# Kernel optimization log

Measured on AMD Instinct MI355X. Metric: run time of the kernel, lower is better.

The kernel has to match this reference:

```python
import jax, jax.numpy as jnp
import numpy as np

N_NODES = 50000
N_EDGES = 400000
NODE_DIM = 128
EDGE_DIM = 64
HIDDEN = 128  # must equal NODE_DIM (index_add into zeros_like(node_feat))
EPS = 1e-8


def _param(key, shape):
    fan_in = shape[0]
    return (jax.random.normal(key, shape, jnp.float32) / np.sqrt(fan_in)).astype(jnp.float32)


def setup_inputs() -> dict:
    key = jax.random.key(0)
    ks = jax.random.split(key, 20)
    inp = {
        'node_feat': jax.random.normal(ks[0], (N_NODES, NODE_DIM), jnp.float32),
        'edge_attr': jax.random.normal(ks[1], (N_EDGES, EDGE_DIM), jnp.float32),
        'coords': 5.0 * jax.random.normal(ks[2], (N_NODES, 3), jnp.float32),
        'edge_index': jax.random.randint(ks[3], (2, N_EDGES), 0, N_NODES, dtype=jnp.int32),
        # edge_mlp: Linear(2*node+edge -> hidden), SiLU, Linear(hidden -> hidden), SiLU
        'We1': _param(ks[4], (2 * NODE_DIM + EDGE_DIM, HIDDEN)),
        'be1': jnp.zeros((HIDDEN,), jnp.float32),
        'We2': _param(ks[5], (HIDDEN, HIDDEN)),
        'be2': jnp.zeros((HIDDEN,), jnp.float32),
        # node_mlp: Linear(node+hidden -> hidden), SiLU, Linear(hidden -> node)
        'Wn1': _param(ks[6], (NODE_DIM + HIDDEN, HIDDEN)),
        'bn1': jnp.zeros((HIDDEN,), jnp.float32),
        'Wn2': _param(ks[7], (HIDDEN, NODE_DIM)),
        'bn2': jnp.zeros((NODE_DIM,), jnp.float32),
        # coord_mlp: Linear(hidden -> hidden//2), SiLU, Linear(hidden//2 -> 1)
        'Wc1': _param(ks[8], (HIDDEN, HIDDEN // 2)),
        'bc1': jnp.zeros((HIDDEN // 2,), jnp.float32),
        'Wc2': _param(ks[9], (HIDDEN // 2, 1)),
        'bc2': jnp.zeros((1,), jnp.float32),
    }
    return inp


def reference(node_feat, edge_attr, coords, edge_index,
              We1, be1, We2, be2,
              Wn1, bn1, Wn2, bn2,
              Wc1, bc1, Wc2, bc2):
    src, dst = edge_index[0], edge_index[1]
    n_nodes = node_feat.shape[0]

    # gather -> edge MLP
    edge_feat = jnp.concatenate([node_feat[src], node_feat[dst], edge_attr], axis=-1)  # [E, 2*ND+ED]
    edge_message = jax.nn.silu(jax.nn.silu(edge_feat @ We1 + be1) @ We2 + be2)         # [E, H]

    # scatter-add messages to destination nodes
    aggr = jax.ops.segment_sum(edge_message, dst, num_segments=n_nodes)                # [N, H]

    # node update (residual)
    node_in = jnp.concatenate([node_feat, aggr], axis=-1)
    node_update = jax.nn.silu(node_in @ Wn1 + bn1) @ Wn2 + bn2
    updated_nodes = node_feat + node_update

    # equivariant coordinate update
    coord_w = jax.nn.silu(edge_message @ Wc1 + bc1) @ Wc2 + bc2                        # [E, 1]
    coord_diff = coords[src] - coords[dst]                                             # [E, 3]
    coord_diff = coord_diff / (jnp.linalg.norm(coord_diff, axis=-1, keepdims=True) + EPS)
    coord_update = jax.ops.segment_sum(coord_w * coord_diff, dst, num_segments=n_nodes)
    updated_coords = coords + coord_update

    return (updated_nodes, updated_coords)
```

## Files before the change

### kernel.cpp

```cpp
#include <hip/hip_runtime.h>
#include <hip/hip_bf16.h>
#include <math.h>
#include <stdint.h>

#define NN 50000
#define NE 400000

typedef __attribute__((ext_vector_type(8))) short short8;
typedef __attribute__((ext_vector_type(4))) float f32x4;

#define OFF_W1S  0
#define OFF_W1D  16384
#define OFF_W1E  32768
#define OFF_WE2T 40960
#define OFF_WN1T 57344
#define OFF_WN2T 90112
#define OFF_WC1T 106496
#define W_TOTAL  114688

__device__ __forceinline__ float silu_f(float x) {
    return x * (1.0f / (1.0f + __expf(-x)));
}
__device__ __forceinline__ short f2bf(float f) {
    __hip_bfloat16 b = __float2bfloat16(f);
    return *reinterpret_cast<short*>(&b);
}
__device__ __forceinline__ float bf2f(short s) {
    uint32_t u = ((uint32_t)(uint16_t)s) << 16;
    float f; __builtin_memcpy(&f, &u, 4); return f;
}
__device__ __forceinline__ short8 cvt8(float4 a, float4 b) {
    short8 r;
    r[0] = f2bf(a.x); r[1] = f2bf(a.y); r[2] = f2bf(a.z); r[3] = f2bf(a.w);
    r[4] = f2bf(b.x); r[5] = f2bf(b.y); r[6] = f2bf(b.z); r[7] = f2bf(b.w);
    return r;
}

__device__ __forceinline__ void gload16(const short* g, short* l) {
    __builtin_amdgcn_global_load_lds(
        (const __attribute__((address_space(1))) void*)g,
        (__attribute__((address_space(3))) void*)l, 16, 0, 0);
}

__global__ void zero_kernel(float4* __restrict__ p, int n4) {
    int i = blockIdx.x * blockDim.x + threadIdx.x;
    int st = gridDim.x * blockDim.x;
    for (; i < n4; i += st) p[i] = make_float4(0.f, 0.f, 0.f, 0.f);
}

__global__ __launch_bounds__(256) void prep_kernel(
    const float* __restrict__ We1, const float* __restrict__ We2,
    const float* __restrict__ Wn1, const float* __restrict__ Wn2,
    const float* __restrict__ Wc1, short* __restrict__ wb)
{
    const int i = blockIdx.x * 256 + threadIdx.x;
    if (i >= W_TOTAL) return;
    float v; int rel, n, k;
    if (i < OFF_W1D)       { rel = i;            n = rel >> 7; k = rel & 127; v = We1[k * 128 + n]; }
    else if (i < OFF_W1E)  { rel = i - OFF_W1D;  n = rel >> 7; k = rel & 127; v = We1[(k + 128) * 128 + n]; }
    else if (i < OFF_WE2T) { rel = i - OFF_W1E;  n = rel >> 6; k = rel & 63;  v = We1[(k + 256) * 128 + n]; }
    else if (i < OFF_WN1T) { rel = i - OFF_WE2T; n = rel >> 7; k = rel & 127; v = We2[k * 128 + n]; }
    else if (i < OFF_WN2T) { rel = i - OFF_WN1T; n = rel >> 8; k = rel & 255; v = Wn1[k * 128 + n]; }
    else if (i < OFF_WC1T) { rel = i - OFF_WN2T; n = rel >> 7; k = rel & 127; v = Wn2[k * 128 + n]; }
    else                   { rel = i - OFF_WC1T; n = rel >> 7; k = rel & 127; v = Wc1[k * 64 + n]; }
    wb[i] = f2bf(v);
}

__global__ __launch_bounds__(256, 4) void ynode_kernel(
    const float* __restrict__ nf, const short* __restrict__ wb,
    short* __restrict__ ysb, short* __restrict__ ydb)
{
    const int tid = threadIdx.x;
    const int wv = tid >> 6, lane = tid & 63, le = lane & 15, grp = lane >> 4;
    const int nb = blockIdx.x * 128, wbase = wv * 32;
    const int row0 = min(nb + wbase + le, NN - 1);
    const int row1 = min(nb + wbase + 16 + le, NN - 1);

    #pragma unroll 1
    for (int pass = 0; pass < 2; ++pass) {
        const short* wt = wb + (pass ? OFF_W1D : OFF_W1S);
        short* op = pass ? ydb : ysb;

        f32x4 acc[2][8];
        #pragma unroll
        for (int m = 0; m < 2; ++m)
            #pragma unroll
            for (int t = 0; t < 8; ++t) acc[m][t] = (f32x4){0.f, 0.f, 0.f, 0.f};

        #pragma unroll
        for (int kc = 0; kc < 4; ++kc) {
            const int gk = kc * 32 + grp * 8;
            const float* p0 = nf + (size_t)row0 * 128 + gk;
            const float* p1 = nf + (size_t)row1 * 128 + gk;
            const short8 a0 = cvt8(*(const float4*)p0, *(const float4*)(p0 + 4));
            const short8 a1 = cvt8(*(const float4*)p1, *(const float4*)(p1 + 4));
            short8 bfv[8];
            #pragma unroll
            for (int t = 0; t < 8; ++t)
                bfv[t] = *(const short8*)(wt + (size_t)(t * 16 + le) * 128 + gk);
            #pragma unroll
            for (int t = 0; t < 8; ++t) {
                acc[0][t] = __builtin_amdgcn_mfma_f32_16x16x32_bf16(a0, bfv[t], acc[0][t], 0, 0, 0);
                acc[1][t] = __builtin_amdgcn_mfma_f32_16x16x32_bf16(a1, bfv[t], acc[1][t], 0, 0, 0);
            }
        }
        #pragma unroll
        for (int t = 0; t < 8; ++t)
            #pragma unroll
            for (int m = 0; m < 2; ++m)
                #pragma unroll
                for (int r = 0; r < 4; ++r) {
                    const int row = nb + wbase + m * 16 + grp * 4 + r;
                    if (row < NN)
                        op[(size_t)row * 128 + t * 16 + le] = f2bf(acc[m][t][r]);
                }
    }
}

__global__ __launch_bounds__(256, 2) void edge_kernel(
    const short* __restrict__ ysb, const short* __restrict__ ydb,
    const float* __restrict__ ea, const float* __restrict__ coords,
    const int* __restrict__ ei, const short* __restrict__ wb,
    const float* __restrict__ be1, const float* __restrict__ be2,
    const float* __restrict__ bc1, const float* __restrict__ bc2,
    const float* __restrict__ Wc2f,
    float* __restrict__ aggr, float* __restrict__ coord_acc)
{
    __shared__ short smem[4][8192];

    const int tid = threadIdx.x;
    const int wv = tid >> 6, lane = tid & 63, le = lane & 15, g = lane >> 4;
    const int base = (blockIdx.x * 4 + wv) * 32;
    short* stage = smem[wv];

    const int s0 = ei[base + le],      s1 = ei[base + 16 + le];
    const int d0 = ei[NE + base + le], d1 = ei[NE + base + 16 + le];

    #pragma unroll
    for (int q = 0; q < 4; ++q) {
        gload16(ysb + (size_t)s0 * 128 + q * 32 + g * 8, stage + q * 512);
        gload16(ysb + (size_t)s1 * 128 + q * 32 + g * 8, stage + 2048 + q * 512);
        gload16(ydb + (size_t)d0 * 128 + q * 32 + g * 8, stage + 4096 + q * 512);
        gload16(ydb + (size_t)d1 * 128 + q * 32 + g * 8, stage + 6144 + q * 512);
    }

    f32x4 acc[2][8];
    #pragma unroll
    for (int m = 0; m < 2; ++m)
        #pragma unroll
        for (int t = 0; t < 8; ++t) acc[m][t] = (f32x4){0.f, 0.f, 0.f, 0.f};

    const short* w1e = wb + OFF_W1E;
    #pragma unroll
    for (int kc = 0; kc < 2; ++kc) {
        const int gk = kc * 32 + g * 8;
        const float* p0 = ea + (size_t)(base + le) * 64 + gk;
        const float* p1 = ea + (size_t)(base + 16 + le) * 64 + gk;
        const short8 a0 = cvt8(*(const float4*)p0, *(const float4*)(p0 + 4));
        const short8 a1 = cvt8(*(const float4*)p1, *(const float4*)(p1 + 4));
        short8 bfv[8];
        #pragma unroll
        for (int t = 0; t < 8; ++t)
            bfv[t] = *(const short8*)(w1e + (size_t)(t * 16 + le) * 64 + gk);
        #pragma unroll
        for (int t = 0; t < 8; ++t) {
            acc[0][t] = __builtin_amdgcn_mfma_f32_16x16x32_bf16(a0, bfv[t], acc[0][t], 0, 0, 0);
            acc[1][t] = __builtin_amdgcn_mfma_f32_16x16x32_bf16(a1, bfv[t], acc[1][t], 0, 0, 0);
        }
    }

    asm volatile("s_waitcnt vmcnt(0)" ::: "memory");
    __builtin_amdgcn_sched_barrier(0);

    #pragma unroll
    for (int t = 0; t < 8; ++t) {
        const int col = t * 16 + le;
        const float b1 = be1[col];
        const int c8 = col >> 3, q = c8 >> 2, cc = c8 & 3, el = col & 7;
        #pragma unroll
        for (int m = 0; m < 2; ++m)
            #pragma unroll
            for (int r = 0; r < 4; ++r) {
                const int ad = m * 2048 + q * 512 + cc * 128 + (g * 4 + r) * 8 + el;
                const float v = silu_f(acc[m][t][r] + bf2f(stage[ad]) + bf2f(stage[4096 + ad]) + b1);
                stage[ad] = f2bf(v);
            }
    }

    f32x4 acc2[2][8];
    #pragma unroll
    for (int m = 0; m < 2; ++m)
        #pragma unroll
        for (int t = 0; t < 8; ++t) acc2[m][t] = (f32x4){0.f, 0.f, 0.f, 0.f};

    const short* w2 = wb + OFF_WE2T;
    #pragma unroll
    for (int kc = 0; kc < 4; ++kc) {
        const int gk = kc * 32 + g * 8;
        const short8 a0 = *(const short8*)&stage[kc * 512 + g * 128 + le * 8];
        const short8 a1 = *(const short8*)&stage[2048 + kc * 512 + g * 128 + le * 8];
        short8 bfv[8];
        #pragma unroll
        for (int t = 0; t < 8; ++t)
            bfv[t] = *(const short8*)(w2 + (size_t)(t * 16 + le) * 128 + gk);
        #pragma unroll
        for (int t = 0; t < 8; ++t) {
            acc2[0][t] = __builtin_amdgcn_mfma_f32_16x16x32_bf16(a0, bfv[t], acc2[0][t], 0, 0, 0);
            acc2[1][t] = __builtin_amdgcn_mfma_f32_16x16x32_bf16(a1, bfv[t], acc2[1][t], 0, 0, 0);
        }
    }

    int dstv[2][4];
    #pragma unroll
    for (int r = 0; r < 4; ++r) {
        dstv[0][r] = __shfl(d0, g * 4 + r);
        dstv[1][r] = __shfl(d1, g * 4 + r);
    }
    #pragma unroll
    for (int t = 0; t < 8; ++t) {
        const int col = t * 16 + le;
        const float b2 = be2[col];
        const int c8 = col >> 3, q = c8 >> 2, cc = c8 & 3, el = col & 7;
        #pragma unroll
        for (int m = 0; m < 2; ++m)
            #pragma unroll
            for (int r = 0; r < 4; ++r) {
                const float v = silu_f(acc2[m][t][r] + b2);
                atomicAdd(&aggr[(size_t)dstv[m][r] * 128 + col], v);
                stage[4096 + m * 2048 + q * 512 + cc * 128 + (g * 4 + r) * 8 + el] = f2bf(v);
            }
    }

    f32x4 acc3[2][4];
    #pragma unroll
    for (int m = 0; m < 2; ++m)
        #pragma unroll
        for (int t = 0; t < 4; ++t) acc3[m][t] = (f32x4){0.f, 0.f, 0.f, 0.f};

    const short* wc = wb + OFF_WC1T;
    #pragma unroll
    for (int kc = 0; kc < 4; ++kc) {
        const int gk = kc * 32 + g * 8;
        const short8 a0 = *(const short8*)&stage[4096 + kc * 512 + g * 128 + le * 8];
        const short8 a1 = *(const short8*)&stage[6144 + kc * 512 + g * 128 + le * 8];
        short8 bfv[4];
        #pragma unroll
        for (int t = 0; t < 4; ++t)
            bfv[t] = *(const short8*)(wc + (size_t)(t * 16 + le) * 128 + gk);
        #pragma unroll
        for (int t = 0; t < 4; ++t) {
            acc3[0][t] = __builtin_amdgcn_mfma_f32_16x16x32_bf16(a0, bfv[t], acc3[0][t], 0, 0, 0);
            acc3[1][t] = __builtin_amdgcn_mfma_f32_16x16x32_bf16(a1, bfv[t], acc3[1][t], 0, 0, 0);
        }
    }

    float part[2][4];
    #pragma unroll
    for (int m = 0; m < 2; ++m)
        #pragma unroll
        for (int r = 0; r < 4; ++r) part[m][r] = 0.f;
    #pragma unroll
    for (int t = 0; t < 4; ++t) {
        const float bc = bc1[t * 16 + le];
        const float w2c = Wc2f[t * 16 + le];
        #pragma unroll
        for (int m = 0; m < 2; ++m)
            #pragma unroll
            for (int r = 0; r < 4; ++r)
                part[m][r] += silu_f(acc3[m][t][r] + bc) * w2c;
    }
    #pragma unroll
    for (int mask = 1; mask <= 8; mask <<= 1)
        #pragma unroll
        for (int m = 0; m < 2; ++m)
            #pragma unroll
            for (int r = 0; r < 4; ++r)
                part[m][r] += __shfl_xor(part[m][r], mask);

    const int rr = le & 3;
    const int sA = __shfl(s0, g * 4 + rr), sB = __shfl(s1, g * 4 + rr);
    const int dA = __shfl(d0, g * 4 + rr), dB = __shfl(d1, g * 4 + rr);

    if (le < 8) {
        const int m = le >> 2, r = le & 3;
        float v;
        if (m == 0) v = (r == 0) ? part[0][0] : (r == 1) ? part[0][1] : (r == 2) ? part[0][2] : part[0][3];
        else        v = (r == 0) ? part[1][0] : (r == 1) ? part[1][1] : (r == 2) ? part[1][2] : part[1][3];
        const int s = m ? sB : sA, d = m ? dB : dA;
        const float dx = coords[3 * s + 0] - coords[3 * d + 0];
        const float dy = coords[3 * s + 1] - coords[3 * d + 1];
        const float dz = coords[3 * s + 2] - coords[3 * d + 2];
        const float wq = v + bc2[0];
        const float inv = wq / (sqrtf(dx * dx + dy * dy + dz * dz) + 1e-8f);
        atomicAdd(&coord_acc[3 * d + 0], dx * inv);
        atomicAdd(&coord_acc[3 * d + 1], dy * inv);
        atomicAdd(&coord_acc[3 * d + 2], dz * inv);
    }
}

__global__ __launch_bounds__(256, 2) void node_kernel(
    const float* __restrict__ nf, const float* __restrict__ coords,
    const short* __restrict__ wb,
    const float* __restrict__ bn1, const float* __restrict__ bn2,
    const float* __restrict__ aggr, const float* __restrict__ coord_acc,
    float* __restrict__ out)
{
    __shared__ short Hs[128][136];

    const int tid = threadIdx.x;
    const int wv = tid >> 6, lane = tid & 63, le = lane & 15, grp = lane >> 4;
    const int nb = blockIdx.x * 128, wbase = wv * 32;
    const int row0 = min(nb + wbase + le, NN - 1);
    const int row1 = min(nb + wbase + 16 + le, NN - 1);

    f32x4 acc[2][8];
    #pragma unroll
    for (int m = 0; m < 2; ++m)
        #pragma unroll
        for (int t = 0; t < 8; ++t) acc[m][t] = (f32x4){0.f, 0.f, 0.f, 0.f};

    const short* w1 = wb + OFF_WN1T;
    #pragma unroll
    for (int kc = 0; kc < 8; ++kc) {
        const int gk = kc * 32 + grp * 8;
        const float* p0 = (kc < 4) ? nf + (size_t)row0 * 128 + gk : aggr + (size_t)row0 * 128 + gk - 128;
        const float* p1 = (kc < 4) ? nf + (size_t)row1 * 128 + gk : aggr + (size_t)row1 * 128 + gk - 128;
        const short8 a0 = cvt8(*(const float4*)p0, *(const float4*)(p0 + 4));
        const short8 a1 = cvt8(*(const float4*)p1, *(const float4*)(p1 + 4));
        short8 bfv[8];
        #pragma unroll
        for (int t = 0; t < 8; ++t)
            bfv[t] = *(const short8*)(w1 + (size_t)(t * 16 + le) * 256 + gk);
        #pragma unroll
        for (int t = 0; t < 8; ++t) {
            acc[0][t] = __builtin_amdgcn_mfma_f32_16x16x32_bf16(a0, bfv[t], acc[0][t], 0, 0, 0);
            acc[1][t] = __builtin_amdgcn_mfma_f32_16x16x32_bf16(a1, bfv[t], acc[1][t], 0, 0, 0);
        }
    }
    #pragma unroll
    for (int t = 0; t < 8; ++t) {
        const float b1 = bn1[t * 16 + le];
        #pragma unroll
        for (int m = 0; m < 2; ++m)
            #pragma unroll
            for (int r = 0; r < 4; ++r)
                Hs[wbase + m * 16 + grp * 4 + r][t * 16 + le] = f2bf(silu_f(acc[m][t][r] + b1));
    }

    f32x4 acc2[2][8];
    #pragma unroll
    for (int m = 0; m < 2; ++m)
        #pragma unroll
        for (int t = 0; t < 8; ++t) acc2[m][t] = (f32x4){0.f, 0.f, 0.f, 0.f};

    const short* w2 = wb + OFF_WN2T;
    #pragma unroll
    for (int kc = 0; kc < 4; ++kc) {
        const int gk = kc * 32 + grp * 8;
        const short8 a0 = *(const short8*)&Hs[wbase + le][gk];
        const short8 a1 = *(const short8*)&Hs[wbase + 16 + le][gk];
        short8 bfv[8];
        #pragma unroll
        for (int t = 0; t < 8; ++t)
            bfv[t] = *(const short8*)(w2 + (size_t)(t * 16 + le) * 128 + gk);
        #pragma unroll
        for (int t = 0; t < 8; ++t) {
            acc2[0][t] = __builtin_amdgcn_mfma_f32_16x16x32_bf16(a0, bfv[t], acc2[0][t], 0, 0, 0);
            acc2[1][t] = __builtin_amdgcn_mfma_f32_16x16x32_bf16(a1, bfv[t], acc2[1][t], 0, 0, 0);
        }
    }
    #pragma unroll
    for (int t = 0; t < 8; ++t) {
        const float b2 = bn2[t * 16 + le];
        #pragma unroll
        for (int m = 0; m < 2; ++m)
            #pragma unroll
            for (int r = 0; r < 4; ++r) {
                const int row = nb + wbase + m * 16 + grp * 4 + r;
                if (row < NN) {
                    const int c = t * 16 + le;
                    out[(size_t)row * 128 + c] = acc2[m][t][r] + b2 + nf[(size_t)row * 128 + c];
                }
            }
    }

    for (int i = tid; i < 384; i += 256) {
        const int n = nb + i / 3, j = i % 3;
        if (n < NN)
            out[(size_t)NN * 128 + 3 * n + j] = coords[3 * n + j] + coord_acc[3 * n + j];
    }
}

extern "C" void kernel_launch(void* const* d_in, const int* in_sizes, int n_in,
                              void* d_out, int out_size, void* d_ws, size_t ws_size,
                              hipStream_t stream)
{
    const float* node_feat  = (const float*)d_in[0];
    const float* edge_attr  = (const float*)d_in[1];
    const float* coords     = (const float*)d_in[2];
    const int*   edge_index = (const int*)d_in[3];
    const float* We1 = (const float*)d_in[4];
    const float* be1 = (const float*)d_in[5];
    const float* We2 = (const float*)d_in[6];
    const float* be2 = (const float*)d_in[7];
    const float* Wn1 = (const float*)d_in[8];
    const float* bn1 = (const float*)d_in[9];
    const float* Wn2 = (const float*)d_in[10];
    const float* bn2 = (const float*)d_in[11];
    const float* Wc1 = (const float*)d_in[12];
    const float* bc1 = (const float*)d_in[13];
    const float* Wc2 = (const float*)d_in[14];
    const float* bc2 = (const float*)d_in[15];
    float* out = (float*)d_out;

    const size_t sz_wb  = (size_t)W_TOTAL * 2;
    const size_t sz_agg = (size_t)NN * 128 * 4;
    const size_t sz_cac = (size_t)NN * 3 * 4;
    const size_t sz_y   = (size_t)NN * 128 * 2;

    char* p = (char*)d_ws;
    short* wbf       = (short*)p;  p += sz_wb;
    float* aggr      = (float*)p;  p += sz_agg;
    float* coord_acc = (float*)p;  p += sz_cac;
    short* ysb       = (short*)p;  p += sz_y;
    short* ydb       = (short*)p;
    (void)ws_size;

    const int n4 = (NN * 128 + NN * 3) / 4;
    const int eg = NE / 128;
    const int ng = (NN + 127) / 128;

    prep_kernel<<<(W_TOTAL + 255) / 256, 256, 0, stream>>>(We1, We2, Wn1, Wn2, Wc1, wbf);
    zero_kernel<<<2048, 256, 0, stream>>>((float4*)aggr, n4);
    ynode_kernel<<<ng, 256, 0, stream>>>(node_feat, wbf, ysb, ydb);

    edge_kernel<<<eg, 256, 0, stream>>>(
        ysb, ydb, edge_attr, coords, edge_index, wbf,
        be1, be2, bc1, bc2, Wc2, aggr, coord_acc);

    node_kernel<<<ng, 256, 0, stream>>>(
        node_feat, coords, wbf, bn1, bn2, aggr, coord_acc, out);
}
```

Baseline: 390.0 us.

## Rewrite edge kernel as register-only transposed MFMA with shuffle exchange, no LDS

The edge kernel now computes the transposed product (weights as the A operand, edge features as B), so each lane owns the columns of one edge. Intermediate activations are passed between the chained matmuls through cross-lane shuffles instead of a shared-memory staging buffer. Each wave now handles 16 edges instead of 32, the grid doubles, and launch bounds allow 4 blocks per SM, removing the LDS round-trips and raising occupancy. The costs are more shuffle instructions, half the reuse of each weight fragment per wave, and aggr atomics that now land on a single destination row per lane with a changed column pattern.

```diff
diff --git a/kernel.cpp b/kernel.cpp
--- a/kernel.cpp
+++ b/kernel.cpp
@@ -29,6 +29,9 @@
     uint32_t u = ((uint32_t)(uint16_t)s) << 16;
     float f; __builtin_memcpy(&f, &u, 4); return f;
 }
+__device__ __forceinline__ uint32_t pk2(float lo, float hi) {
+    return (uint32_t)(uint16_t)f2bf(lo) | ((uint32_t)(uint16_t)f2bf(hi) << 16);
+}
 __device__ __forceinline__ short8 cvt8(float4 a, float4 b) {
     short8 r;
     r[0] = f2bf(a.x); r[1] = f2bf(a.y); r[2] = f2bf(a.z); r[3] = f2bf(a.w);
@@ -36,10 +39,20 @@
     return r;
 }
 
-__device__ __forceinline__ void gload16(const short* g, short* l) {
-    __builtin_amdgcn_global_load_lds(
-        (const __attribute__((address_space(1))) void*)g,
-        (__attribute__((address_space(3))) void*)l, 16, 0, 0);
+__device__ __forceinline__ short8 exch8(uint32_t e0, uint32_t e1,
+                                        uint32_t o0, uint32_t o1,
+                                        int g, int le) {
+    const int srcA = le + 16 * ((g & 1) * 2);
+    const int srcB = srcA + 16;
+    const uint32_t a0e = __shfl((int)e0, srcA), a0o = __shfl((int)o0, srcA);
+    const uint32_t a1e = __shfl((int)e1, srcA), a1o = __shfl((int)o1, srcA);
+    const uint32_t b0e = __shfl((int)e0, srcB), b0o = __shfl((int)o0, srcB);
+    const uint32_t b1e = __shfl((int)e1, srcB), b1o = __shfl((int)o1, srcB);
+    const bool hi = (g & 2) != 0;
+    uint32_t v[4];
+    v[0] = hi ? a0o : a0e;  v[1] = hi ? a1o : a1e;
+    v[2] = hi ? b0o : b0e;  v[3] = hi ? b1o : b1e;
+    short8 r; __builtin_memcpy(&r, v, 16); return r;
 }
 
 __global__ void zero_kernel(float4* __restrict__ p, int n4) {
@@ -117,7 +130,7 @@
     }
 }
 
-__global__ __launch_bounds__(256, 2) void edge_kernel(
+__global__ __launch_bounds__(256, 4) void edge_kernel(
     const short* __restrict__ ysb, const short* __restrict__ ydb,
     const float* __restrict__ ea, const float* __restrict__ coords,
     const int* __restrict__ ei, const short* __restrict__ wb,
@@ -126,175 +139,134 @@
     const float* __restrict__ Wc2f,
     float* __restrict__ aggr, float* __restrict__ coord_acc)
 {
-    __shared__ short smem[4][8192];
-
     const int tid = threadIdx.x;
     const int wv = tid >> 6, lane = tid & 63, le = lane & 15, g = lane >> 4;
-    const int base = (blockIdx.x * 4 + wv) * 32;
-    short* stage = smem[wv];
-
-    const int s0 = ei[base + le],      s1 = ei[base + 16 + le];
-    const int d0 = ei[NE + base + le], d1 = ei[NE + base + 16 + le];
-
-    #pragma unroll
-    for (int q = 0; q < 4; ++q) {
-        gload16(ysb + (size_t)s0 * 128 + q * 32 + g * 8, stage + q * 512);
-        gload16(ysb + (size_t)s1 * 128 + q * 32 + g * 8, stage + 2048 + q * 512);
-        gload16(ydb + (size_t)d0 * 128 + q * 32 + g * 8, stage + 4096 + q * 512);
-        gload16(ydb + (size_t)d1 * 128 + q * 32 + g * 8, stage + 6144 + q * 512);
-    }
-
-    f32x4 acc[2][8];
-    #pragma unroll
-    for (int m = 0; m < 2; ++m)
-        #pragma unroll
-        for (int t = 0; t < 8; ++t) acc[m][t] = (f32x4){0.f, 0.f, 0.f, 0.f};
+    const int e = (blockIdx.x * 4 + wv) * 16 + le;
+
+    const int s0 = ei[e], d0 = ei[NE + e];
+
+    short8 ys8[4], yd8[4];
+    #pragma unroll
+    for (int cc = 0; cc < 4; ++cc) {
+        ys8[cc] = *(const short8*)(ysb + (size_t)s0 * 128 + cc * 32 + g * 8);
+        yd8[cc] = *(const short8*)(ydb + (size_t)d0 * 128 + cc * 32 + g * 8);
+    }
+
+    short8 eaB[2];
+    #pragma unroll
+    for (int kc = 0; kc < 2; ++kc) {
+        const float* pe = ea + (size_t)e * 64 + kc * 32 + g * 8;
+        eaB[kc] = cvt8(*(const float4*)pe, *(const float4*)(pe + 4));
+    }
+
+    f32x4 acc[8];
+    #pragma unroll
+    for (int t = 0; t < 8; ++t) acc[t] = (f32x4){0.f, 0.f, 0.f, 0.f};
 
     const short* w1e = wb + OFF_W1E;
     #pragma unroll
     for (int kc = 0; kc < 2; ++kc) {
         const int gk = kc * 32 + g * 8;
-        const float* p0 = ea + (size_t)(base + le) * 64 + gk;
-        const float* p1 = ea + (size_t)(base + 16 + le) * 64 + gk;
-        const short8 a0 = cvt8(*(const float4*)p0, *(const float4*)(p0 + 4));
-        const short8 a1 = cvt8(*(const float4*)p1, *(const float4*)(p1 + 4));
-        short8 bfv[8];
-        #pragma unroll
-        for (int t = 0; t < 8; ++t)
-            bfv[t] = *(const short8*)(w1e + (size_t)(t * 16 + le) * 64 + gk);
-        #pragma unroll
-        for (int t = 0; t < 8; ++t) {
-            acc[0][t] = __builtin_amdgcn_mfma_f32_16x16x32_bf16(a0, bfv[t], acc[0][t], 0, 0, 0);
-            acc[1][t] = __builtin_amdgcn_mfma_f32_16x16x32_bf16(a1, bfv[t], acc[1][t], 0, 0, 0);
+        short8 wfv[8];
+        #pragma unroll
+        for (int t = 0; t < 8; ++t)
+            wfv[t] = *(const short8*)(w1e + (size_t)(t * 16 + le) * 64 + gk);
+        #pragma unroll
+        for (int t = 0; t < 8; ++t)
+            acc[t] = __builtin_amdgcn_mfma_f32_16x16x32_bf16(wfv[t], eaB[kc], acc[t], 0, 0, 0);
+    }
+
+    uint32_t hp[8][2];
+    #pragma unroll
+    for (int t = 0; t < 8; ++t) {
+        hp[t][0] = pk2(acc[t][0], acc[t][1]);
+        hp[t][1] = pk2(acc[t][2], acc[t][3]);
+    }
+
+    short8 h1f[4];
+    #pragma unroll
+    for (int cc = 0; cc < 4; ++cc) {
+        const short8 ex = exch8(hp[cc*2][0], hp[cc*2][1], hp[cc*2+1][0], hp[cc*2+1][1], g, le);
+        const float* bp = be1 + cc * 32 + g * 8;
+        #pragma unroll
+        for (int j = 0; j < 8; ++j)
+            h1f[cc][j] = f2bf(silu_f(bf2f(ex[j]) + bf2f(ys8[cc][j]) + bf2f(yd8[cc][j]) + bp[j]));
+    }
+
+    f32x4 acc2[8];
+    #pragma unroll
+    for (int t = 0; t < 8; ++t) acc2[t] = (f32x4){0.f, 0.f, 0.f, 0.f};
+
+    const short* w2 = wb + OFF_WE2T;
+    #pragma unroll
+    for (int cc = 0; cc < 4; ++cc) {
+        const int gk = cc * 32 + g * 8;
+        short8 wfv[8];
+        #pragma unroll
+        for (int t = 0; t < 8; ++t)
+            wfv[t] = *(const short8*)(w2 + (size_t)(t * 16 + le) * 128 + gk);
+        #pragma unroll
+        for (int t = 0; t < 8; ++t)
+            acc2[t] = __builtin_amdgcn_mfma_f32_16x16x32_bf16(wfv[t], h1f[cc], acc2[t], 0, 0, 0);
+    }
+
+    uint32_t hq[8][2];
+    #pragma unroll
+    for (int t = 0; t < 8; ++t) {
+        float hv[4];
+        #pragma unroll
+        for (int r = 0; r < 4; ++r) {
+            const int col = t * 16 + g * 4 + r;
+            const float v = silu_f(acc2[t][r] + be2[col]);
+            hv[r] = v;
+            atomicAdd(&aggr[(size_t)d0 * 128 + col], v);
         }
-    }
-
-    asm volatile("s_waitcnt vmcnt(0)" ::: "memory");
-    __builtin_amdgcn_sched_barrier(0);
-
-    #pragma unroll
-    for (int t = 0; t < 8; ++t) {
-        const int col = t * 16 + le;
-        const float b1 = be1[col];
-        const int c8 = col >> 3, q = c8 >> 2, cc = c8 & 3, el = col & 7;
-        #pragma unroll
-        for (int m = 0; m < 2; ++m)
-            #pragma unroll
-            for (int r = 0; r < 4; ++r) {
-                const int ad = m * 2048 + q * 512 + cc * 128 + (g * 4 + r) * 8 + el;
-                const float v = silu_f(acc[m][t][r] + bf2f(stage[ad]) + bf2f(stage[4096 + ad]) + b1);
-                stage[ad] = f2bf(v);
-            }
-    }
-
-    f32x4 acc2[2][8];
-    #pragma unroll
-    for (int m = 0; m < 2; ++m)
-        #pragma unroll
-        for (int t = 0; t < 8; ++t) acc2[m][t] = (f32x4){0.f, 0.f, 0.f, 0.f};
-
-    const short* w2 = wb + OFF_WE2T;
-    #pragma unroll
-    for (int kc = 0; kc < 4; ++kc) {
-        const int gk = kc * 32 + g * 8;
-        const short8 a0 = *(const short8*)&stage[kc * 512 + g * 128 + le * 8];
-        const short8 a1 = *(const short8*)&stage[2048 + kc * 512 + g * 128 + le * 8];
-        short8 bfv[8];
-        #pragma unroll
-        for (int t = 0; t < 8; ++t)
-            bfv[t] = *(const short8*)(w2 + (size_t)(t * 16 + le) * 128 + gk);
-        #pragma unroll
-        for (int t = 0; t < 8; ++t) {
-            acc2[0][t] = __builtin_amdgcn_mfma_f32_16x16x32_bf16(a0, bfv[t], acc2[0][t], 0, 0, 0);
-            acc2[1][t] = __builtin_amdgcn_mfma_f32_16x16x32_bf16(a1, bfv[t], acc2[1][t], 0, 0, 0);
+        hq[t][0] = pk2(hv[0], hv[1]);
+        hq[t][1] = pk2(hv[2], hv[3]);
+    }
+
+    short8 h2f[4];
+    #pragma unroll
+    for (int cc = 0; cc < 4; ++cc)
+        h2f[cc] = exch8(hq[cc*2][0], hq[cc*2][1], hq[cc*2+1][0], hq[cc*2+1][1], g, le);
+
+    f32x4 acc3[4];
+    #pragma unroll
+    for (int t = 0; t < 4; ++t) acc3[t] = (f32x4){0.f, 0.f, 0.f, 0.f};
+
+    const short* wc = wb + OFF_WC1T;
+    #pragma unroll
+    for (int cc = 0; cc < 4; ++cc) {
+        const int gk = cc * 32 + g * 8;
+        short8 wfv[4];
+        #pragma unroll
+        for (int t = 0; t < 4; ++t)
+            wfv[t] = *(const short8*)(wc + (size_t)(t * 16 + le) * 128 + gk);
+        #pragma unroll
+        for (int t = 0; t < 4; ++t)
+            acc3[t] = __builtin_amdgcn_mfma_f32_16x16x32_bf16(wfv[t], h2f[cc], acc3[t], 0, 0, 0);
+    }
+
+    float part = 0.f;
+    #pragma unroll
+    for (int t = 0; t < 4; ++t)
+        #pragma unroll
+        for (int r = 0; r < 4; ++r) {
+            const int col = t * 16 + g * 4 + r;
+            part += silu_f(acc3[t][r] + bc1[col]) * Wc2f[col];
         }
-    }
-
-    int dstv[2][4];
-    #pragma unroll
-    for (int r = 0; r < 4; ++r) {
-        dstv[0][r] = __shfl(d0, g * 4 + r);
-        dstv[1][r] = __shfl(d1, g * 4 + r);
-    }
-    #pragma unroll
-    for (int t = 0; t < 8; ++t) {
-        const int col = t * 16 + le;
-        const float b2 = be2[col];
-        const int c8 = col >> 3, q = c8 >> 2, cc = c8 & 3, el = col & 7;
-        #pragma unroll
-        for (int m = 0; m < 2; ++m)
-            #pragma unroll
-            for (int r = 0; r < 4; ++r) {
-                const float v = silu_f(acc2[m][t][r] + b2);
-                atomicAdd(&aggr[(size_t)dstv[m][r] * 128 + col], v);
-                stage[4096 + m * 2048 + q * 512 + cc * 128 + (g * 4 + r) * 8 + el] = f2bf(v);
-            }
-    }
-
-    f32x4 acc3[2][4];
-    #pragma unroll
-    for (int m = 0; m < 2; ++m)
-        #pragma unroll
-        for (int t = 0; t < 4; ++t) acc3[m][t] = (f32x4){0.f, 0.f, 0.f, 0.f};
-
-    const short* wc = wb + OFF_WC1T;
-    #pragma unroll
-    for (int kc = 0; kc < 4; ++kc) {
-        const int gk = kc * 32 + g * 8;
-        const short8 a0 = *(const short8*)&stage[4096 + kc * 512 + g * 128 + le * 8];
-        const short8 a1 = *(const short8*)&stage[6144 + kc * 512 + g * 128 + le * 8];
-        short8 bfv[4];
-        #pragma unroll
-        for (int t = 0; t < 4; ++t)
-            bfv[t] = *(const short8*)(wc + (size_t)(t * 16 + le) * 128 + gk);
-        #pragma unroll
-        for (int t = 0; t < 4; ++t) {
-            acc3[0][t] = __builtin_amdgcn_mfma_f32_16x16x32_bf16(a0, bfv[t], acc3[0][t], 0, 0, 0);
-            acc3[1][t] = __builtin_amdgcn_mfma_f32_16x16x32_bf16(a1, bfv[t], acc3[1][t], 0, 0, 0);
-        }
-    }
-
-    float part[2][4];
-    #pragma unroll
-    for (int m = 0; m < 2; ++m)
-        #pragma unroll
-        for (int r = 0; r < 4; ++r) part[m][r] = 0.f;
-    #pragma unroll
-    for (int t = 0; t < 4; ++t) {
-        const float bc = bc1[t * 16 + le];
-        const float w2c = Wc2f[t * 16 + le];
-        #pragma unroll
-        for (int m = 0; m < 2; ++m)
-            #pragma unroll
-            for (int r = 0; r < 4; ++r)
-                part[m][r] += silu_f(acc3[m][t][r] + bc) * w2c;
-    }
-    #pragma unroll
-    for (int mask = 1; mask <= 8; mask <<= 1)
-        #pragma unroll
-        for (int m = 0; m < 2; ++m)
-            #pragma unroll
-            for (int r = 0; r < 4; ++r)
-                part[m][r] += __shfl_xor(part[m][r], mask);
-
-    const int rr = le & 3;
-    const int sA = __shfl(s0, g * 4 + rr), sB = __shfl(s1, g * 4 + rr);
-    const int dA = __shfl(d0, g * 4 + rr), dB = __shfl(d1, g * 4 + rr);
-
-    if (le < 8) {
-        const int m = le >> 2, r = le & 3;
-        float v;
-        if (m == 0) v = (r == 0) ? part[0][0] : (r == 1) ? part[0][1] : (r == 2) ? part[0][2] : part[0][3];
-        else        v = (r == 0) ? part[1][0] : (r == 1) ? part[1][1] : (r == 2) ? part[1][2] : part[1][3];
-        const int s = m ? sB : sA, d = m ? dB : dA;
-        const float dx = coords[3 * s + 0] - coords[3 * d + 0];
-        const float dy = coords[3 * s + 1] - coords[3 * d + 1];
-        const float dz = coords[3 * s + 2] - coords[3 * d + 2];
-        const float wq = v + bc2[0];
+    part += __shfl_xor(part, 16);
+    part += __shfl_xor(part, 32);
+
+    if (g == 0) {
+        const float wq = part + bc2[0];
+        const float dx = coords[3 * s0 + 0] - coords[3 * d0 + 0];
+        const float dy = coords[3 * s0 + 1] - coords[3 * d0 + 1];
+        const float dz = coords[3 * s0 + 2] - coords[3 * d0 + 2];
         const float inv = wq / (sqrtf(dx * dx + dy * dy + dz * dz) + 1e-8f);
-        atomicAdd(&coord_acc[3 * d + 0], dx * inv);
-        atomicAdd(&coord_acc[3 * d + 1], dy * inv);
-        atomicAdd(&coord_acc[3 * d + 2], dz * inv);
+        atomicAdd(&coord_acc[3 * d0 + 0], dx * inv);
+        atomicAdd(&coord_acc[3 * d0 + 1], dy * inv);
+        atomicAdd(&coord_acc[3 * d0 + 2], dz * inv);
     }
 }
 
@@ -427,7 +399,7 @@
     (void)ws_size;
 
     const int n4 = (NN * 128 + NN * 3) / 4;
-    const int eg = NE / 128;
+    const int eg = NE / 64;
     const int ng = (NN + 127) / 128;
 
     prep_kernel<<<(W_TOTAL + 255) / 256, 256, 0, stream>>>(We1, We2, Wn1, Wn2, Wc1, wbf);
```

After: 861.4 us. +120.9%, slower.
